# Kernel optimization log

Measured on AMD Instinct MI355X. Metric: run time of the kernel, lower is better.

Reference implementation:

```python
import jax, jax.numpy as jnp
import numpy as np

N_POINTS = 65536      # total nodes across the batch
NDIMS = 3
NUM_THETAS = 64       # directions
BUMP_STEPS = 32       # discretization steps of [-radius, radius]
NUM_GRAPHS = 64       # number of point clouds in the batch
RADIUS = 1.1
SCALE = 100.0         # sigmoid sharpness


def setup_inputs() -> dict:
    key = jax.random.key(0)
    k1, k2, k3 = jax.random.split(key, 3)
    x = jax.random.normal(k1, (N_POINTS, NDIMS), dtype=jnp.float32)
    # unit-norm direction vectors on the sphere, columns of v: [ndims, num_thetas]
    v = jax.random.normal(k2, (NDIMS, NUM_THETAS), dtype=jnp.float32)
    v = v / jnp.linalg.norm(v, axis=0, keepdims=True)
    # lin = discretization of [-radius, radius], matches nn.Parameter linspace
    lin = jnp.linspace(-RADIUS, RADIUS, BUMP_STEPS, dtype=jnp.float32)
    # sorted batch index assigning each node to a graph (torch_geometric convention)
    batch = jnp.sort(jax.random.randint(k3, (N_POINTS,), 0, NUM_GRAPHS, dtype=jnp.int32))
    return {"x": x, "v": v, "lin": lin, "batch": batch}


def reference(x, v, lin, batch):
    # node heights: inner product of coordinates with each direction -> [N, T]
    nh = x @ v
    # broadcast soft-threshold: sigmoid(scale * (lin - nh)) -> [N, S, T]
    # (torch builds [S,1,N,T] then movedims to [N,1,S,T]; same values)
    ecc = jax.nn.sigmoid(SCALE * (lin[None, :, None] - nh[:, None, :]))
    # segment scatter-add over nodes per graph -> [B, S, T]
    ect = jax.ops.segment_sum(ecc, batch, num_segments=NUM_GRAPHS)
    return ect  # torch output after .squeeze(): [batch, bump_steps, num_thetas]
```

## Files before the change

### kernel.cpp

```cpp
#include <hip/hip_runtime.h>

#define T      64
#define S      32
#define NGRAPH 64
#define NSPLIT 16
#define NW     4

__global__ __launch_bounds__(256, 4) void ect_partial(
    const float* __restrict__ x, const float* __restrict__ v,
    const float* __restrict__ lin, const int* __restrict__ batch,
    float* __restrict__ ws, int n_points)
{
    __shared__ float bins[256 * 34];

    const int tid  = threadIdx.x;
    const int t    = tid & 63;
    const int w    = tid >> 6;
    const int b    = blockIdx.x;
    const int g    = b >> 4;
    const int c    = b & (NSPLIT - 1);

    {
        const float4 z4 = {0.0f, 0.0f, 0.0f, 0.0f};
        float4* b4 = (float4*)bins;
        for (int i = tid; i < 256 * 34 / 4; i += 256) b4[i] = z4;
    }

    const int target = (t < 32) ? g : (g + 1);
    const int i32    = t & 31;
    int lo = 0;
    const int strides[3] = {2048, 64, 2};
#pragma unroll
    for (int rnd = 0; rnd < 3; rnd++) {
        const int stride = strides[rnd];
        const int idx  = lo + i32 * stride;
        const int pv   = batch[min(idx, n_points - 1)];
        const bool prd = (idx < n_points) && (pv < target);
        const unsigned long long bal = __ballot(prd);
        const int cnt = __popc((unsigned)(bal >> (t & 32)));
        lo += max(cnt - 1, 0) * stride;
    }
#pragma unroll
    for (int rnd = 0; rnd < 2; rnd++) {
        const int idx = min(lo, n_points - 1);
        if ((lo < n_points) && (batch[idx] < target)) lo++;
    }
    const int gstart = __builtin_amdgcn_readfirstlane(lo);
    const int gend   = __builtin_amdgcn_readlane(lo, 32);
    const int len    = gend - gstart;
    const int n0     = gstart + (len * c) / NSPLIT;
    const int n1     = gstart + (len * (c + 1)) / NSPLIT;

    const float lin0     = lin[0];
    const float step     = lin[1] - lin0;
    const float inv_step = 1.0f / step;
    const float nl0i     = -lin0 * inv_step;
    const float K2 = (100.0f * step) * 1.4426950408889634f;
    const float r  = __builtin_amdgcn_exp2f(-K2);

    const float v0 = v[0 * T + t];
    const float v1 = v[1 * T + t];
    const float v2 = v[2 * T + t];

    float v0acc = 0.0f;
    const int binb = tid * 34;
    __syncthreads();

#pragma unroll 2
    for (int n = n0 + w; n < n1; n += NW) {
        const float x0 = x[3 * n + 0];
        const float x1 = x[3 * n + 1];
        const float x2 = x[3 * n + 2];
        const float nh = fmaf(x0, v0, fmaf(x1, v1, x2 * v2));
        const float f  = fmaf(nh, inv_step, nl0i);
        const float fs = ceilf(f);
        const int   ss = (int)fs;
        const float e0 = __builtin_amdgcn_exp2f(fmaf(K2, f - fs, K2));
        const float e1 = e0 * r;
        const float sm  = __builtin_amdgcn_rcpf(1.0f + e0);
        const float s0v = __builtin_amdgcn_rcpf(1.0f + e1);
        v0acc += (ss <= -1) ? 1.0f : (ss == 0 ? s0v : (ss == 1 ? sm : 0.0f));
        const int p0 = ss - 1, p1 = ss, p2 = ss + 1;
        const int a0 = binb + (((unsigned)(p0 - 1) < 31u) ? p0 : 33);
        const int a1 = binb + (((unsigned)(p1 - 1) < 31u) ? p1 : 33);
        const int a2 = binb + (((unsigned)(p2 - 1) < 31u) ? p2 : 33);
        const float r0 = bins[a0], r1 = bins[a1], r2 = bins[a2];
        bins[a0] = r0 + sm;
        bins[a1] = r1 + (s0v - sm);
        bins[a2] = r2 + (1.0f - s0v);
    }

    bins[binb + 0] = v0acc;
    __syncthreads();

    for (int cell = tid; cell < 32 * 64; cell += 256) {
        const int cc = cell >> 6;
        const int tt = cell & 63;
        const float sum = bins[(  0 + tt) * 34 + cc] + bins[( 64 + tt) * 34 + cc]
                        + bins[(128 + tt) * 34 + cc] + bins[(192 + tt) * 34 + cc];
        bins[tt * 34 + cc] = sum;
    }
    __syncthreads();

    float run = bins[t * 34 + 0];
    const int sbase = 8 * w;
    for (int cc = 1; cc < sbase; cc++) run += bins[t * 34 + cc];
    float* wsb = ws + (size_t)b * (S * T);
#pragma unroll
    for (int j = 0; j < 8; j++) {
        const int s = sbase + j;
        if (s >= 1) run += bins[t * 34 + s];
        wsb[s * T + t] = run;
    }
}

__global__ __launch_bounds__(256) void ect_reduce(
    const float* __restrict__ ws, float* __restrict__ out)
{
    const int idx = blockIdx.x * 256 + threadIdx.x;
    const int g   = idx >> 11;
    const int i   = idx & 2047;
    float sum = 0.0f;
#pragma unroll
    for (int c = 0; c < NSPLIT; c++)
        sum += ws[(size_t)(g * NSPLIT + c) * (S * T) + i];
    out[idx] = sum;
}

extern "C" void kernel_launch(void* const* d_in, const int* in_sizes, int n_in,
                              void* d_out, int out_size, void* d_ws, size_t ws_size,
                              hipStream_t stream) {
    const float* x     = (const float*)d_in[0];
    const float* v     = (const float*)d_in[1];
    const float* lin   = (const float*)d_in[2];
    const int*   batch = (const int*)d_in[3];
    float* out = (float*)d_out;
    float* ws  = (float*)d_ws;

    const int n_points = in_sizes[0] / 3;

    ect_partial<<<NGRAPH * NSPLIT, 256, 0, stream>>>(x, v, lin, batch, ws, n_points);
    ect_reduce<<<NGRAPH * S * T / 256, 256, 0, stream>>>(ws, out);
}
```

Measured before the change: 74.18 us.

## Fuse partial and reduce kernels into one block per graph

Drops the 16-way per-graph split and the second reduction kernel. Each graph is now handled by a single block that writes its cumulative bins straight to the output. This removes the workspace write and read and one kernel launch. The trade-off is only 64 blocks on the device, so each block processes a whole graph serially with much lower parallelism. The binary-search refinement is also trimmed from two increment steps to one.

```diff
diff --git a/kernel.cpp b/kernel.cpp
--- a/kernel.cpp
+++ b/kernel.cpp
@@ -3,22 +3,19 @@
 #define T      64
 #define S      32
 #define NGRAPH 64
-#define NSPLIT 16
 #define NW     4
 
-__global__ __launch_bounds__(256, 4) void ect_partial(
+__global__ __launch_bounds__(256, 2) void ect_fused(
     const float* __restrict__ x, const float* __restrict__ v,
     const float* __restrict__ lin, const int* __restrict__ batch,
-    float* __restrict__ ws, int n_points)
+    float* __restrict__ out, int n_points)
 {
     __shared__ float bins[256 * 34];
 
-    const int tid  = threadIdx.x;
-    const int t    = tid & 63;
-    const int w    = tid >> 6;
-    const int b    = blockIdx.x;
-    const int g    = b >> 4;
-    const int c    = b & (NSPLIT - 1);
+    const int tid = threadIdx.x;
+    const int t   = tid & 63;
+    const int w   = tid >> 6;
+    const int g   = blockIdx.x;
 
     {
         const float4 z4 = {0.0f, 0.0f, 0.0f, 0.0f};
@@ -40,16 +37,9 @@
         const int cnt = __popc((unsigned)(bal >> (t & 32)));
         lo += max(cnt - 1, 0) * stride;
     }
-#pragma unroll
-    for (int rnd = 0; rnd < 2; rnd++) {
-        const int idx = min(lo, n_points - 1);
-        if ((lo < n_points) && (batch[idx] < target)) lo++;
-    }
-    const int gstart = __builtin_amdgcn_readfirstlane(lo);
-    const int gend   = __builtin_amdgcn_readlane(lo, 32);
-    const int len    = gend - gstart;
-    const int n0     = gstart + (len * c) / NSPLIT;
-    const int n1     = gstart + (len * (c + 1)) / NSPLIT;
+    if ((lo < n_points) && (batch[min(lo, n_points - 1)] < target)) lo++;
+    const int n0 = __builtin_amdgcn_readfirstlane(lo);
+    const int n1 = __builtin_amdgcn_readlane(lo, 32);
 
     const float lin0     = lin[0];
     const float step     = lin[1] - lin0;
@@ -105,26 +95,13 @@
     float run = bins[t * 34 + 0];
     const int sbase = 8 * w;
     for (int cc = 1; cc < sbase; cc++) run += bins[t * 34 + cc];
-    float* wsb = ws + (size_t)b * (S * T);
+    float* og = out + g * (S * T);
 #pragma unroll
     for (int j = 0; j < 8; j++) {
         const int s = sbase + j;
         if (s >= 1) run += bins[t * 34 + s];
-        wsb[s * T + t] = run;
+        og[s * T + t] = run;
     }
-}
-
-__global__ __launch_bounds__(256) void ect_reduce(
-    const float* __restrict__ ws, float* __restrict__ out)
-{
-    const int idx = blockIdx.x * 256 + threadIdx.x;
-    const int g   = idx >> 11;
-    const int i   = idx & 2047;
-    float sum = 0.0f;
-#pragma unroll
-    for (int c = 0; c < NSPLIT; c++)
-        sum += ws[(size_t)(g * NSPLIT + c) * (S * T) + i];
-    out[idx] = sum;
 }
 
 extern "C" void kernel_launch(void* const* d_in, const int* in_sizes, int n_in,
@@ -135,10 +112,8 @@
     const float* lin   = (const float*)d_in[2];
     const int*   batch = (const int*)d_in[3];
     float* out = (float*)d_out;
-    float* ws  = (float*)d_ws;
 
     const int n_points = in_sizes[0] / 3;
 
-    ect_partial<<<NGRAPH * NSPLIT, 256, 0, stream>>>(x, v, lin, batch, ws, n_points);
-    ect_reduce<<<NGRAPH * S * T / 256, 256, 0, stream>>>(ws, out);
+    ect_fused<<<NGRAPH, 256, 0, stream>>>(x, v, lin, batch, out, n_points);
 }
```

Result: slower. 119.9 us (+61.6%).
